# Kernel tuning notes

Measured on AMD Instinct MI355X. Metric: run time of the kernel, lower is better.

Reference implementation:

```python
import jax, jax.numpy as jnp
import numpy as np

MODEL_DIM = 2048
NUM_HEADS = 16
NUM_KV_HEADS = 4
HEAD_DIM = MODEL_DIM // NUM_HEADS  # 128
ROPE_BASE = 10000.0
LOCAL_WINDOW = 1024
EPS = 1.1920929e-07  # torch.finfo(float32).eps, F.rms_norm default
NEG = -1e30


def setup_inputs() -> dict:
    key = jax.random.key(0)
    ks = jax.random.split(key, 5)
    s = 0.02
    return {
        "x": jax.random.normal(ks[0], (1, 4096, MODEL_DIM), jnp.float32),
        "Wq": jax.random.normal(ks[1], (MODEL_DIM, MODEL_DIM), jnp.float32) * s,
        "Wk": jax.random.normal(ks[2], (NUM_KV_HEADS * HEAD_DIM, MODEL_DIM), jnp.float32) * s,
        "Wv": jax.random.normal(ks[3], (NUM_KV_HEADS * HEAD_DIM, MODEL_DIM), jnp.float32) * s,
        "Wo": jax.random.normal(ks[4], (MODEL_DIM, MODEL_DIM), jnp.float32) * s,
    }


def _rms_norm(x):
    return x * jax.lax.rsqrt(jnp.mean(x * x, axis=-1, keepdims=True) + EPS)


def _rope_tables(seqlen, dtype):
    inv_freq = 1.0 / (ROPE_BASE ** (jnp.arange(0, HEAD_DIM, 2, dtype=jnp.float32) / HEAD_DIM))
    freqs = jnp.arange(seqlen, dtype=jnp.float32)[:, None] * inv_freq[None, :]  # [S, hd/2]
    return jnp.cos(freqs).astype(dtype), jnp.sin(freqs).astype(dtype)


def _apply_rope(x, cos, sin):
    # x: [B, H, S, hd]; cos/sin: [S, hd/2]
    half = x.shape[-1] // 2
    x1, x2 = x[..., :half], x[..., half:]
    c = cos[None, None, :, :]
    s = sin[None, None, :, :]
    return jnp.concatenate((x1 * c + x2 * s, x2 * c - x1 * s), axis=-1)


def reference(x, Wq, Wk, Wv, Wo):
    B, S, _ = x.shape
    G = NUM_HEADS // NUM_KV_HEADS
    q = (x @ Wq.T).reshape(B, S, NUM_HEADS, HEAD_DIM).transpose(0, 2, 1, 3)
    k = (x @ Wk.T).reshape(B, S, NUM_KV_HEADS, HEAD_DIM).transpose(0, 2, 1, 3)
    v = (x @ Wv.T).reshape(B, S, NUM_KV_HEADS, HEAD_DIM).transpose(0, 2, 1, 3)
    q = _rms_norm(q)
    k = _rms_norm(k)
    cos, sin = _rope_tables(S, q.dtype)
    q = _apply_rope(q, cos, sin)
    k = _apply_rope(k, cos, sin)
    # GQA: expand kv heads to match query heads
    k = jnp.repeat(k, G, axis=1)  # [B, H, S, hd]
    v = jnp.repeat(v, G, axis=1)
    scale = 1.0 / np.sqrt(HEAD_DIM)
    scores = jnp.einsum("bhqd,bhkd->bhqk", q, k) * scale  # [B, H, S, S]
    idx = jnp.arange(S)
    causal = idx[None, :] <= idx[:, None]
    in_window = idx[None, :] > idx[:, None] - LOCAL_WINDOW
    allowed = causal & in_window  # [S, S]
    scores = jnp.where(allowed[None, None, :, :], scores, NEG)
    probs = jax.nn.softmax(scores, axis=-1)
    y = jnp.einsum("bhqk,bhkd->bhqd", probs, v)  # [B, H, S, hd]
    y = y.transpose(0, 2, 1, 3).reshape(B, S, MODEL_DIM)
    return y @ Wo.T
```

## Files before the change

### kernel.cpp

```cpp
#include <hip/hip_runtime.h>

typedef short bf16x8 __attribute__((ext_vector_type(8)));
typedef float f32x4 __attribute__((ext_vector_type(4)));

__device__ __forceinline__ ushort f2b(float f) {
  union { float f; unsigned u; } v; v.f = f;
  unsigned r = v.u + 0x7FFF + ((v.u >> 16) & 1);
  return (ushort)(r >> 16);
}
__device__ __forceinline__ float b2f(ushort u) {
  union { unsigned u; float f; } v; v.u = ((unsigned)u) << 16;
  return v.f;
}
__device__ __forceinline__ unsigned cvtpk(float lo, float hi) {
  unsigned r;
  asm volatile("v_cvt_pk_bf16_f32 %0, %1, %2" : "=v"(r) : "v"(lo), "v"(hi));
  return r;
}
__device__ __forceinline__ f32x4 mfma16(bf16x8 a, bf16x8 b, f32x4 c) {
  return __builtin_amdgcn_mfma_f32_16x16x32_bf16(a, b, c, 0, 0, 0);
}

#define GLD_LDS16(g, l) \
  __builtin_amdgcn_global_load_lds((const __attribute__((address_space(1))) void*)(g), \
                                   (__attribute__((address_space(3))) void*)(l), 16, 0, 0)

__global__ __launch_bounds__(256) void cast_all(const float* __restrict__ x,
                                                const float* __restrict__ wq,
                                                const float* __restrict__ wk,
                                                const float* __restrict__ wv,
                                                const float* __restrict__ wo,
                                                ushort* __restrict__ xb,
                                                ushort* __restrict__ wqkvb,
                                                ushort* __restrict__ wob) {
  const long i = (long)blockIdx.x * 256 + threadIdx.x;
  const float* src;
  ushort* dst;
  long j;
  if (i < 2097152) {
    src = x; j = i; dst = xb;
  } else if (i < 3145728) {
    src = wq; j = i - 2097152; dst = wqkvb;
  } else if (i < 3407872) {
    src = wk; j = i - 3145728; dst = wqkvb + 4194304;
  } else if (i < 3670016) {
    src = wv; j = i - 3407872; dst = wqkvb + 5242880;
  } else {
    src = wo; j = i - 3670016; dst = wob;
  }
  float4 f = ((const float4*)src)[j];
  ushort4 u;
  u.x = f2b(f.x); u.y = f2b(f.y); u.z = f2b(f.z); u.w = f2b(f.w);
  ((ushort4*)dst)[j] = u;
}

__global__ void rope_tables_k(float* __restrict__ cosT, float* __restrict__ sinT) {
  int s = blockIdx.x, i = threadIdx.x;
  float inv = powf(10000.0f, -(float)i * (1.0f / 64.0f));
  float f = (float)s * inv;
  cosT[s * 64 + i] = cosf(f);
  sinT[s * 64 + i] = sinf(f);
}

template <int BM, int BN, bool BF16OUT>
__global__ __launch_bounds__(512, 2) void gemm8p(const ushort* __restrict__ A,
                                                 const ushort* __restrict__ B,
                                                 void* __restrict__ Cout,
                                                 int M, int N, int K) {
  constexpr int AF = BM / 64;
  constexpr int BF = BN / 64;
  constexpr int MFR = BM / 32;
  constexpr int LA = BM / 128;
  constexpr int LB = BN / 128;
  constexpr int ASZ = BM * 32;
  constexpr int BSZ = BN * 32;
  constexpr int VMN = LA + 2 * LB;
  __shared__ __align__(16) ushort lds[4 * (ASZ + BSZ)];
  const int t = threadIdx.x;
  const int lane = t & 63, w = t >> 6;
  const int wr = w & 1, wc = w >> 1;
  const int l15 = lane & 15, l4 = lane >> 4;
  const int nbn = N / BN;
  const int nwg = (int)gridDim.x;
  int bid = (int)blockIdx.x;
  bid = (bid & 7) * (nwg >> 3) + (bid >> 3);
  const long m0 = (long)(bid / nbn) * BM;
  const long n0 = (long)(bid % nbn) * BN;
  const int nk = K >> 6;
  const int rdl = l15 * 32 + ((l4 ^ ((l15 >> 1) & 3)) * 8);

  f32x4 acc[MFR][BF] = {};
  bf16x8 af[AF], bf[BF];

#define STA(tile, ks)                                                          \
  do {                                                                         \
    const int tt_ = (tile) < nk ? (tile) : nk - 1;                             \
    _Pragma("unroll") for (int c = 0; c < LA; ++c) {                           \
      const int us_ = t * 8 + c * 4096;                                        \
      const int r_ = us_ >> 5;                                                 \
      const int cs_ = (((us_ >> 3) & 3) ^ ((r_ >> 1) & 3)) * 8;                \
      GLD_LDS16(A + (m0 + r_) * K + tt_ * 64 + (ks) * 32 + cs_,                \
                &lds[(((tile) & 1) * 2 + (ks)) * ASZ + us_]);                  \
    }                                                                          \
  } while (0)
#define STB(tile, ks)                                                          \
  do {                                                                         \
    const int tt_ = (tile) < nk ? (tile) : nk - 1;                             \
    _Pragma("unroll") for (int c = 0; c < LB; ++c) {                           \
      const int us_ = t * 8 + c * 4096;                                        \
      const int r_ = us_ >> 5;                                                 \
      const int cs_ = (((us_ >> 3) & 3) ^ ((r_ >> 1) & 3)) * 8;                \
      GLD_LDS16(B + (n0 + r_) * K + tt_ * 64 + (ks) * 32 + cs_,                \
                &lds[4 * ASZ + (((tile) & 1) * 2 + (ks)) * BSZ + us_]);        \
    }                                                                          \
  } while (0)
#define LDA8(slot, ks, mq)                                                     \
  _Pragma("unroll") for (int a = 0; a < AF; ++a)                               \
      af[a] = *(const bf16x8*)(&lds[((slot) * 2 + (ks)) * ASZ +                \
                                    (wr * MFR + (mq) * AF + a) * 512 + rdl]);
#define LDB8(slot, ks)                                                         \
  _Pragma("unroll") for (int b = 0; b < BF; ++b)                               \
      bf[b] = *(const bf16x8*)(&lds[4 * ASZ + ((slot) * 2 + (ks)) * BSZ +      \
                                    (wc * BF + b) * 512 + rdl]);
#define VMW()                                                                  \
  do {                                                                         \
    if constexpr (VMN == 7)                                                    \
      asm volatile("s_waitcnt vmcnt(7)" ::: "memory");                         \
    else if constexpr (VMN == 6)                                               \
      asm volatile("s_waitcnt vmcnt(6)" ::: "memory");                         \
    else                                                                       \
      asm volatile("s_waitcnt vmcnt(5)" ::: "memory");                         \
  } while (0)
#define BARMM(mq)                                                              \
  do {                                                                         \
    __builtin_amdgcn_s_barrier();                                              \
    asm volatile("s_waitcnt lgkmcnt(0)" ::: "memory");                         \
    __builtin_amdgcn_sched_barrier(0);                                         \
    __builtin_amdgcn_s_setprio(1);                                             \
    _Pragma("unroll") for (int a = 0; a < AF; ++a)                             \
        _Pragma("unroll") for (int b = 0; b < BF; ++b)                         \
            acc[(mq) * AF + a][b] = mfma16(af[a], bf[b], acc[(mq) * AF + a][b]); \
    __builtin_amdgcn_s_setprio(0);                                             \
    __builtin_amdgcn_s_barrier();                                              \
  } while (0)

  STA(0, 0); STB(0, 0); STA(0, 1); STB(0, 1);
  STA(1, 0); STB(1, 0); STB(1, 1);
  VMW();
  __builtin_amdgcn_s_barrier();

  for (int i = 0; i < (nk >> 1); ++i) {
    const int t1 = 2 * i + 1, t2 = 2 * i + 2, t3 = 2 * i + 3;
    LDA8(0, 0, 0); LDB8(0, 0); STA(t1, 1);          BARMM(0);
    LDA8(0, 0, 1);             STB(t2, 0);          BARMM(1);
    LDA8(0, 1, 0); LDB8(0, 1); STA(t2, 0);          BARMM(0);
    LDA8(0, 1, 1);             STB(t2, 1); VMW();   BARMM(1);
    LDA8(1, 0, 0); LDB8(1, 0); STA(t2, 1);          BARMM(0);
    LDA8(1, 0, 1);             STB(t3, 0);          BARMM(1);
    LDA8(1, 1, 0); LDB8(1, 1); STA(t3, 0);          BARMM(0);
    LDA8(1, 1, 1);             STB(t3, 1); VMW();   BARMM(1);
  }
  asm volatile("s_waitcnt vmcnt(0)" ::: "memory");

#pragma unroll
  for (int m = 0; m < MFR; ++m) {
#pragma unroll
    for (int n = 0; n < BF; ++n) {
      long mrow = m0 + wr * (BM / 2) + m * 16 + l4 * 4;
      long ncol = n0 + wc * (BN / 4) + n * 16 + l15;
#pragma unroll
      for (int r = 0; r < 4; ++r) {
        if constexpr (BF16OUT)
          ((ushort*)Cout)[(mrow + r) * N + ncol] = f2b(acc[m][n][r]);
        else
          ((float*)Cout)[(mrow + r) * N + ncol] = acc[m][n][r];
      }
    }
  }
#undef STA
#undef STB
#undef LDA8
#undef LDB8
#undef VMW
#undef BARMM
}

__global__ __launch_bounds__(256) void postproc_k(const ushort* __restrict__ qkvb,
                                                  const float* __restrict__ cosT,
                                                  const float* __restrict__ sinT,
                                                  ushort* __restrict__ qb,
                                                  ushort* __restrict__ kb,
                                                  ushort* __restrict__ vtb) {
  const int lane = threadIdx.x & 63;
  const int s = blockIdx.x * 4 + (threadIdx.x >> 6);
  const int h = blockIdx.y;
  const int colbase = (h < 16) ? h * 128 : (h < 20 ? 2048 + (h - 16) * 128
                                                   : 2560 + (h - 20) * 128);
  const ushort* row = qkvb + (long)s * 3072 + colbase;
  float x1 = b2f(row[lane]), x2 = b2f(row[lane + 64]);
  if (h >= 20) {
    int kvh = h - 20;
    int spos = (s & ~31) | (((s >> 2) & 3) * 8 + ((s >> 4) & 1) * 4 + (s & 3));
    vtb[(long)(kvh * 128 + lane) * 4096 + spos]      = f2b(x1);
    vtb[(long)(kvh * 128 + lane + 64) * 4096 + spos] = f2b(x2);
    return;
  }
  float ss = x1 * x1 + x2 * x2;
#pragma unroll
  for (int m = 1; m < 64; m <<= 1) ss += __shfl_xor(ss, m);
  float rn = rsqrtf(ss * (1.0f / 128.0f) + 1.1920929e-07f);
  float c = cosT[s * 64 + lane], sn = sinT[s * 64 + lane];
  float x1n = x1 * rn, x2n = x2 * rn;
  float o1 = x1n * c + x2n * sn;
  float o2 = x2n * c - x1n * sn;
  if (h < 16) {
    const float scq = 0.08838834764831845f;
    ushort* dst = qb + ((long)h * 4096 + s) * 128;
    dst[lane] = f2b(o1 * scq);
    dst[lane + 64] = f2b(o2 * scq);
  } else {
    ushort* dst = kb + ((long)(h - 16) * 4096 + s) * 128;
    dst[lane] = f2b(o1);
    dst[lane + 64] = f2b(o2);
  }
}

__global__ __launch_bounds__(256, 2) void attn_k(const ushort* __restrict__ qb,
                                                 const ushort* __restrict__ kb,
                                                 const ushort* __restrict__ vtb,
                                                 ushort* __restrict__ yb) {
  __shared__ __align__(16) ushort lds[32768];
  const int t = threadIdx.x;
  const int lane = t & 63, w = t >> 6;
  const int l15 = lane & 15, l4 = lane >> 4;
  const int q0 = ((int)gridDim.x - 1 - (int)blockIdx.x) * 128;
  const int h = blockIdx.y, kvh = h >> 2;
  const int qw = q0 + w * 32;
  const int qA = qw + l15, qB = qw + 16 + l15;
  const int lrd = l15 * 32 + ((l4 ^ ((l15 >> 1) & 3)) * 8);

  bf16x8 qf0[4], qf1[4];
  {
    const ushort* QpA = qb + ((long)h * 4096 + qA) * 128 + l4 * 8;
    const ushort* QpB = qb + ((long)h * 4096 + qB) * 128 + l4 * 8;
#pragma unroll
    for (int c = 0; c < 4; ++c) {
      qf0[c] = *(const bf16x8*)(QpA + c * 32);
      qf1[c] = *(const bf16x8*)(QpB + c * 32);
    }
  }

  const ushort* Kg = kb + (long)kvh * 4096 * 128;
  const ushort* Vg = vtb + (long)kvh * 128 * 4096;

  int kb_lo = q0 - 1023; if (kb_lo < 0) kb_lo = 0; kb_lo &= ~63;
  const int nt = (q0 + 127 - kb_lo) / 64 + 1;

#define STAGE(kbs, b)                                                          \
  do {                                                                         \
    ushort* L_ = &lds[(b) * 16384];                                            \
    _Pragma("unroll") for (int c = 0; c < 8; ++c) {                            \
      const int us_ = t * 8 + c * 2048;                                        \
      if (c < 4) {                                                             \
        const int r_ = (us_ >> 5) & 63;                                        \
        const int cs_ = (((us_ >> 3) & 3) ^ ((r_ >> 1) & 3)) * 8;              \
        GLD_LDS16(Kg + (long)((kbs) + r_) * 128 + (us_ >> 11) * 32 + cs_,      \
                  L_ + us_);                                                   \
      } else {                                                                 \
        const int uv_ = us_ - 8192;                                            \
        const int r_ = (uv_ >> 5) & 127;                                       \
        const int cs_ = (((uv_ >> 3) & 3) ^ ((r_ >> 1) & 3)) * 8;              \
        GLD_LDS16(Vg + (long)r_ * 4096 + (kbs) + (uv_ >> 12) * 32 + cs_,       \
                  L_ + us_);                                                   \
      }                                                                        \
    }                                                                          \
  } while (0)

#define SMAX(sg, mr, lr, og, PA, PB)                                           \
  do {                                                                         \
    float mx = fmaxf(fmaxf(fmaxf(sg[0], sg[1]), fmaxf(sg[2], sg[3])),          \
                     fmaxf(fmaxf(sg[4], sg[5]), fmaxf(sg[6], sg[7])));         \
    mx = fmaxf(mx, fmaxf(fmaxf(fmaxf(sg[8], sg[9]), fmaxf(sg[10], sg[11])),    \
                         fmaxf(fmaxf(sg[12], sg[13]), fmaxf(sg[14], sg[15]))));\
    mx = fmaxf(mx, __shfl_xor(mx, 16));                                        \
    mx = fmaxf(mx, __shfl_xor(mx, 32));                                        \
    float mn;                                                                  \
    if (__all(mx <= (mr) + 8.0f)) {                                            \
      mn = (mr);                                                               \
    } else {                                                                   \
      mn = fmaxf((mr), mx);                                                    \
      const float corr = __expf((mr)-mn);                                      \
      (mr) = mn;                                                               \
      _Pragma("unroll") for (int db = 0; db < 8; ++db)                         \
          _Pragma("unroll") for (int r = 0; r < 4; ++r) og[db][r] *= corr;     \
      (lr) *= corr;                                                            \
    }                                                                          \
    float p[16];                                                               \
    _Pragma("unroll") for (int j = 0; j < 16; ++j) p[j] = __expf(sg[j] - mn);  \
    float ps = ((p[0] + p[1]) + (p[2] + p[3])) + ((p[4] + p[5]) + (p[6] + p[7])); \
    ps += ((p[8] + p[9]) + (p[10] + p[11])) + ((p[12] + p[13]) + (p[14] + p[15])); \
    ps += __shfl_xor(ps, 16);                                                  \
    ps += __shfl_xor(ps, 32);                                                  \
    (lr) += ps;                                                                \
    PA.u[0] = cvtpk(p[0], p[1]);   PA.u[1] = cvtpk(p[2], p[3]);                \
    PA.u[2] = cvtpk(p[4], p[5]);   PA.u[3] = cvtpk(p[6], p[7]);                \
    PB.u[0] = cvtpk(p[8], p[9]);   PB.u[1] = cvtpk(p[10], p[11]);              \
    PB.u[2] = cvtpk(p[12], p[13]); PB.u[3] = cvtpk(p[14], p[15]);              \
  } while (0)

  f32x4 o0[8] = {}, o1[8] = {};
  float mr0 = -1e30f, lr0 = 0.0f, mr1 = -1e30f, lr1 = 0.0f;

  STAGE(kb_lo, 0);

  for (int ti = 0; ti < nt; ++ti) {
    const int kbs = kb_lo + ti * 64;
    const int cur = ti & 1;
    const int tn = (ti + 1 < nt) ? ti + 1 : nt - 1;
    STAGE(kb_lo + tn * 64, cur ^ 1);
    asm volatile("s_waitcnt vmcnt(8)" ::: "memory");
    __builtin_amdgcn_s_barrier();

    if (kbs <= qw + 31 && kbs + 63 >= qw - 1023) {
      const ushort* Kl = &lds[cur * 16384];
      const ushort* Vl = Kl + 8192;

      f32x4 sc0[4], sc1[4];
#pragma unroll
      for (int st = 0; st < 4; ++st) {
        sc0[st] = f32x4{0.f, 0.f, 0.f, 0.f};
        sc1[st] = f32x4{0.f, 0.f, 0.f, 0.f};
#pragma unroll
        for (int c = 0; c < 4; ++c) {
          bf16x8 kf = *(const bf16x8*)(Kl + c * 2048 + st * 512 + lrd);
          sc0[st] = mfma16(kf, qf0[c], sc0[st]);
          sc1[st] = mfma16(kf, qf1[c], sc1[st]);
        }
      }

      float s0[16], s1[16];
      const bool fullA = (kbs + 64 <= qw) && (kbs >= qw - 1008);
      const bool fullB = (kbs + 64 <= qw + 16) && (kbs >= qw - 992);
      if (fullA) {
#pragma unroll
        for (int st = 0; st < 4; ++st)
#pragma unroll
          for (int r = 0; r < 4; ++r) s0[st * 4 + r] = sc0[st][r];
      } else {
#pragma unroll
        for (int st = 0; st < 4; ++st)
#pragma unroll
          for (int r = 0; r < 4; ++r) {
            const int ki = kbs + st * 16 + l4 * 4 + r;
            s0[st * 4 + r] = (ki <= qA && ki > qA - 1024) ? sc0[st][r] : -1e30f;
          }
      }
      if (fullB) {
#pragma unroll
        for (int st = 0; st < 4; ++st)
#pragma unroll
          for (int r = 0; r < 4; ++r) s1[st * 4 + r] = sc1[st][r];
      } else {
#pragma unroll
        for (int st = 0; st < 4; ++st)
#pragma unroll
          for (int r = 0; r < 4; ++r) {
            const int ki = kbs + st * 16 + l4 * 4 + r;
            s1[st * 4 + r] = (ki <= qB && ki > qB - 1024) ? sc1[st][r] : -1e30f;
          }
      }

      union { unsigned u[4]; bf16x8 v; } pa0, pb0, pa1, pb1;
      SMAX(s0, mr0, lr0, o0, pa0, pb0);
      SMAX(s1, mr1, lr1, o1, pa1, pb1);

#pragma unroll
      for (int db = 0; db < 8; ++db) {
        bf16x8 v0 = *(const bf16x8*)(Vl + db * 512 + lrd);
        o0[db] = mfma16(v0, pa0.v, o0[db]);
        o1[db] = mfma16(v0, pa1.v, o1[db]);
        bf16x8 v1 = *(const bf16x8*)(Vl + 4096 + db * 512 + lrd);
        o0[db] = mfma16(v1, pb0.v, o0[db]);
        o1[db] = mfma16(v1, pb1.v, o1[db]);
      }
    }
    __builtin_amdgcn_s_barrier();
  }

  const float i0 = 1.0f / lr0, i1 = 1.0f / lr1;
#pragma unroll
  for (int db = 0; db < 8; ++db)
#pragma unroll
    for (int r = 0; r < 4; ++r) {
      yb[(long)qA * 2048 + h * 128 + db * 16 + l4 * 4 + r] = f2b(o0[db][r] * i0);
      yb[(long)qB * 2048 + h * 128 + db * 16 + l4 * 4 + r] = f2b(o1[db][r] * i1);
    }
#undef STAGE
#undef SMAX
}

extern "C" void kernel_launch(void* const* d_in, const int* in_sizes, int n_in,
                              void* d_out, int out_size, void* d_ws, size_t ws_size,
                              hipStream_t stream) {
  (void)in_sizes; (void)n_in; (void)out_size; (void)ws_size;
  const float* x  = (const float*)d_in[0];
  const float* Wq = (const float*)d_in[1];
  const float* Wk = (const float*)d_in[2];
  const float* Wv = (const float*)d_in[3];
  const float* Wo = (const float*)d_in[4];
  const long S = 4096;
  ushort* ws   = (ushort*)d_ws;
  ushort* xb   = ws;
  ushort* wqkv = xb + S * 2048;
  ushort* wob  = wqkv + 3072L * 2048;
  ushort* qkvb = wob + 2048L * 2048;
  ushort* qb   = qkvb + S * 3072;
  ushort* kbuf = qb + S * 2048;
  ushort* vtb  = kbuf + 4L * 4096 * 128;
  ushort* yb   = vtb + 4L * 128 * 4096;
  float* cosT  = (float*)(yb + S * 2048);
  float* sinT  = cosT + S * 64;

  cast_all<<<dim3(18432), 256, 0, stream>>>(x, Wq, Wk, Wv, Wo, xb, wqkv, wob);
  gemm8p<128, 384, true><<<dim3(256), 512, 0, stream>>>(xb, wqkv, qkvb, 4096, 3072, 2048);
  rope_tables_k<<<dim3(4096), 64, 0, stream>>>(cosT, sinT);
  postproc_k<<<dim3(1024, 24), 256, 0, stream>>>(qkvb, cosT, sinT, qb, kbuf, vtb);
  attn_k<<<dim3(32, 16), 256, 0, stream>>>(qb, kbuf, vtb, yb);
  gemm8p<128, 256, false><<<dim3(256), 512, 0, stream>>>(yb, wob, d_out, 4096, 2048, 2048);
}
```

Measured before the change: 191.0 us.

## Enlarge attention query tile to 256 rows, four 16-row groups per wave

Each attention block now covers 256 query rows instead of 128, and each wave handles four 16-row query groups instead of two. Every K/V tile staged into LDS is reused by twice as many queries, which halves the K/V global traffic and the LDS reads per query. The grid shrinks from 512 to 256 blocks, and the per-thread accumulator and Q-fragment registers double. The launch bound drops its 2-blocks-per-SM hint, so occupancy and load balance across the mi355x's CUs may suffer.

```diff
diff --git a/kernel.cpp b/kernel.cpp
--- a/kernel.cpp
+++ b/kernel.cpp
@@ -225,36 +225,32 @@
   }
 }
 
-__global__ __launch_bounds__(256, 2) void attn_k(const ushort* __restrict__ qb,
-                                                 const ushort* __restrict__ kb,
-                                                 const ushort* __restrict__ vtb,
-                                                 ushort* __restrict__ yb) {
+__global__ __launch_bounds__(256) void attn_k(const ushort* __restrict__ qb,
+                                              const ushort* __restrict__ kb,
+                                              const ushort* __restrict__ vtb,
+                                              ushort* __restrict__ yb) {
   __shared__ __align__(16) ushort lds[32768];
   const int t = threadIdx.x;
   const int lane = t & 63, w = t >> 6;
   const int l15 = lane & 15, l4 = lane >> 4;
-  const int q0 = ((int)gridDim.x - 1 - (int)blockIdx.x) * 128;
+  const int q0 = ((int)gridDim.x - 1 - (int)blockIdx.x) * 256;
   const int h = blockIdx.y, kvh = h >> 2;
-  const int qw = q0 + w * 32;
-  const int qA = qw + l15, qB = qw + 16 + l15;
+  const int qw = q0 + w * 64;
   const int lrd = l15 * 32 + ((l4 ^ ((l15 >> 1) & 3)) * 8);
 
-  bf16x8 qf0[4], qf1[4];
-  {
-    const ushort* QpA = qb + ((long)h * 4096 + qA) * 128 + l4 * 8;
-    const ushort* QpB = qb + ((long)h * 4096 + qB) * 128 + l4 * 8;
-#pragma unroll
-    for (int c = 0; c < 4; ++c) {
-      qf0[c] = *(const bf16x8*)(QpA + c * 32);
-      qf1[c] = *(const bf16x8*)(QpB + c * 32);
-    }
+  bf16x8 qf[4][4];
+#pragma unroll
+  for (int g = 0; g < 4; ++g) {
+    const ushort* Qp = qb + ((long)h * 4096 + qw + g * 16 + l15) * 128 + l4 * 8;
+#pragma unroll
+    for (int c = 0; c < 4; ++c) qf[g][c] = *(const bf16x8*)(Qp + c * 32);
   }
 
   const ushort* Kg = kb + (long)kvh * 4096 * 128;
   const ushort* Vg = vtb + (long)kvh * 128 * 4096;
 
   int kb_lo = q0 - 1023; if (kb_lo < 0) kb_lo = 0; kb_lo &= ~63;
-  const int nt = (q0 + 127 - kb_lo) / 64 + 1;
+  const int nt = (q0 + 255 - kb_lo) / 64 + 1;
 
 #define STAGE(kbs, b)                                                          \
   do {                                                                         \
@@ -276,7 +272,7 @@
     }                                                                          \
   } while (0)
 
-#define SMAX(sg, mr, lr, og, PA, PB)                                           \
+#define SMAX(sg, mr_, lr_, og, PA, PB)                                         \
   do {                                                                         \
     float mx = fmaxf(fmaxf(fmaxf(sg[0], sg[1]), fmaxf(sg[2], sg[3])),          \
                      fmaxf(fmaxf(sg[4], sg[5]), fmaxf(sg[6], sg[7])));         \
@@ -285,15 +281,15 @@
     mx = fmaxf(mx, __shfl_xor(mx, 16));                                        \
     mx = fmaxf(mx, __shfl_xor(mx, 32));                                        \
     float mn;                                                                  \
-    if (__all(mx <= (mr) + 8.0f)) {                                            \
-      mn = (mr);                                                               \
+    if (__all(mx <= (mr_) + 8.0f)) {                                           \
+      mn = (mr_);                                                              \
     } else {                                                                   \
-      mn = fmaxf((mr), mx);                                                    \
-      const float corr = __expf((mr)-mn);                                      \
-      (mr) = mn;                                                               \
+      mn = fmaxf((mr_), mx);                                                   \
+      const float corr = __expf((mr_)-mn);                                     \
+      (mr_) = mn;                                                              \
       _Pragma("unroll") for (int db = 0; db < 8; ++db)                         \
           _Pragma("unroll") for (int r = 0; r < 4; ++r) og[db][r] *= corr;     \
-      (lr) *= corr;                                                            \
+      (lr_) *= corr;                                                           \
     }                                                                          \
     float p[16];                                                               \
     _Pragma("unroll") for (int j = 0; j < 16; ++j) p[j] = __expf(sg[j] - mn);  \
@@ -301,15 +297,18 @@
     ps += ((p[8] + p[9]) + (p[10] + p[11])) + ((p[12] + p[13]) + (p[14] + p[15])); \
     ps += __shfl_xor(ps, 16);                                                  \
     ps += __shfl_xor(ps, 32);                                                  \
-    (lr) += ps;                                                                \
+    (lr_) += ps;                                                               \
     PA.u[0] = cvtpk(p[0], p[1]);   PA.u[1] = cvtpk(p[2], p[3]);                \
     PA.u[2] = cvtpk(p[4], p[5]);   PA.u[3] = cvtpk(p[6], p[7]);                \
     PB.u[0] = cvtpk(p[8], p[9]);   PB.u[1] = cvtpk(p[10], p[11]);              \
     PB.u[2] = cvtpk(p[12], p[13]); PB.u[3] = cvtpk(p[14], p[15]);              \
   } while (0)
 
-  f32x4 o0[8] = {}, o1[8] = {};
-  float mr0 = -1e30f, lr0 = 0.0f, mr1 = -1e30f, lr1 = 0.0f;
+  f32x4 o[4][8] = {};
+  float mr[4], lr[4];
+#pragma unroll
+  for (int g = 0; g < 4; ++g) { mr[g] = -1e30f; lr[g] = 0.0f; }
+  union PU { unsigned u[4]; bf16x8 v; };
 
   STAGE(kb_lo, 0);
 
@@ -321,80 +320,72 @@
     asm volatile("s_waitcnt vmcnt(8)" ::: "memory");
     __builtin_amdgcn_s_barrier();
 
-    if (kbs <= qw + 31 && kbs + 63 >= qw - 1023) {
+    if (kbs <= qw + 63 && kbs + 63 >= qw - 1023) {
       const ushort* Kl = &lds[cur * 16384];
       const ushort* Vl = Kl + 8192;
 
-      f32x4 sc0[4], sc1[4];
+      f32x4 sc[4][4];
+#pragma unroll
+      for (int g = 0; g < 4; ++g)
+#pragma unroll
+        for (int st = 0; st < 4; ++st) sc[g][st] = f32x4{0.f, 0.f, 0.f, 0.f};
 #pragma unroll
       for (int st = 0; st < 4; ++st) {
-        sc0[st] = f32x4{0.f, 0.f, 0.f, 0.f};
-        sc1[st] = f32x4{0.f, 0.f, 0.f, 0.f};
 #pragma unroll
         for (int c = 0; c < 4; ++c) {
           bf16x8 kf = *(const bf16x8*)(Kl + c * 2048 + st * 512 + lrd);
-          sc0[st] = mfma16(kf, qf0[c], sc0[st]);
-          sc1[st] = mfma16(kf, qf1[c], sc1[st]);
+#pragma unroll
+          for (int g = 0; g < 4; ++g) sc[g][st] = mfma16(kf, qf[g][c], sc[g][st]);
         }
       }
 
-      float s0[16], s1[16];
-      const bool fullA = (kbs + 64 <= qw) && (kbs >= qw - 1008);
-      const bool fullB = (kbs + 64 <= qw + 16) && (kbs >= qw - 992);
-      if (fullA) {
-#pragma unroll
-        for (int st = 0; st < 4; ++st)
-#pragma unroll
-          for (int r = 0; r < 4; ++r) s0[st * 4 + r] = sc0[st][r];
-      } else {
-#pragma unroll
-        for (int st = 0; st < 4; ++st)
-#pragma unroll
-          for (int r = 0; r < 4; ++r) {
-            const int ki = kbs + st * 16 + l4 * 4 + r;
-            s0[st * 4 + r] = (ki <= qA && ki > qA - 1024) ? sc0[st][r] : -1e30f;
-          }
+      PU pa[4], pb[4];
+#pragma unroll
+      for (int g = 0; g < 4; ++g) {
+        const int qg0 = qw + g * 16;
+        const int qg = qg0 + l15;
+        float s[16];
+        if ((kbs + 64 <= qg0) && (kbs >= qg0 - 1008)) {
+#pragma unroll
+          for (int st = 0; st < 4; ++st)
+#pragma unroll
+            for (int r = 0; r < 4; ++r) s[st * 4 + r] = sc[g][st][r];
+        } else {
+#pragma unroll
+          for (int st = 0; st < 4; ++st)
+#pragma unroll
+            for (int r = 0; r < 4; ++r) {
+              const int ki = kbs + st * 16 + l4 * 4 + r;
+              s[st * 4 + r] = (ki <= qg && ki > qg - 1024) ? sc[g][st][r] : -1e30f;
+            }
+        }
+        SMAX(s, mr[g], lr[g], o[g], pa[g], pb[g]);
       }
-      if (fullB) {
-#pragma unroll
-        for (int st = 0; st < 4; ++st)
-#pragma unroll
-          for (int r = 0; r < 4; ++r) s1[st * 4 + r] = sc1[st][r];
-      } else {
-#pragma unroll
-        for (int st = 0; st < 4; ++st)
-#pragma unroll
-          for (int r = 0; r < 4; ++r) {
-            const int ki = kbs + st * 16 + l4 * 4 + r;
-            s1[st * 4 + r] = (ki <= qB && ki > qB - 1024) ? sc1[st][r] : -1e30f;
-          }
-      }
-
-      union { unsigned u[4]; bf16x8 v; } pa0, pb0, pa1, pb1;
-      SMAX(s0, mr0, lr0, o0, pa0, pb0);
-      SMAX(s1, mr1, lr1, o1, pa1, pb1);
 
 #pragma unroll
       for (int db = 0; db < 8; ++db) {
         bf16x8 v0 = *(const bf16x8*)(Vl + db * 512 + lrd);
-        o0[db] = mfma16(v0, pa0.v, o0[db]);
-        o1[db] = mfma16(v0, pa1.v, o1[db]);
         bf16x8 v1 = *(const bf16x8*)(Vl + 4096 + db * 512 + lrd);
-        o0[db] = mfma16(v1, pb0.v, o0[db]);
-        o1[db] = mfma16(v1, pb1.v, o1[db]);
+#pragma unroll
+        for (int g = 0; g < 4; ++g) {
+          o[g][db] = mfma16(v0, pa[g].v, o[g][db]);
+          o[g][db] = mfma16(v1, pb[g].v, o[g][db]);
+        }
       }
     }
     __builtin_amdgcn_s_barrier();
   }
 
-  const float i0 = 1.0f / lr0, i1 = 1.0f / lr1;
-#pragma unroll
-  for (int db = 0; db < 8; ++db)
-#pragma unroll
-    for (int r = 0; r < 4; ++r) {
-      yb[(long)qA * 2048 + h * 128 + db * 16 + l4 * 4 + r] = f2b(o0[db][r] * i0);
-      yb[(long)qB * 2048 + h * 128 + db * 16 + l4 * 4 + r] = f2b(o1[db][r] * i1);
-    }
+#pragma unroll
+  for (int g = 0; g < 4; ++g) {
+    const float inv = 1.0f / lr[g];
+    const long qrow = qw + g * 16 + l15;
+#pragma unroll
+    for (int db = 0; db < 8; ++db)
+#pragma unroll
+      for (int r = 0; r < 4; ++r)
+        yb[qrow * 2048 + h * 128 + db * 16 + l4 * 4 + r] = f2b(o[g][db][r] * inv);
+  }
 #undef STAGE
 #undef SMAX
 }
@@ -425,6 +416,6 @@
   gemm8p<128, 384, true><<<dim3(256), 512, 0, stream>>>(xb, wqkv, qkvb, 4096, 3072, 2048);
   rope_tables_k<<<dim3(4096), 64, 0, stream>>>(cosT, sinT);
   postproc_k<<<dim3(1024, 24), 256, 0, stream>>>(qkvb, cosT, sinT, qb, kbuf, vtb);
-  attn_k<<<dim3(32, 16), 256, 0, stream>>>(qb, kbuf, vtb, yb);
+  attn_k<<<dim3(16, 16), 256, 0, stream>>>(qb, kbuf, vtb, yb);
   gemm8p<128, 256, false><<<dim3(256), 512, 0, stream>>>(yb, wob, d_out, 4096, 2048, 2048);
 }
```

New measurement: 224.3 us. 1.17x slower.

## Load V fragments directly from global memory instead of staging through LDS

Applied to the files above, without the earlier changes.

Only K tiles are now staged in LDS, which halves the shared buffer. Each wave loads its V^T fragments straight from global memory into registers, and the loads are interleaved with the softmax to hide their latency. The launch-bounds occupancy hint is dropped and the vmcnt wait is lowered to match the smaller staging. Every wave now fetches the same V data separately, so global/L2 traffic and register pressure go up in exchange for lower LDS usage and fewer LDS reads.

```diff
diff --git a/kernel.cpp b/kernel.cpp
--- a/kernel.cpp
+++ b/kernel.cpp
@@ -225,11 +225,11 @@
   }
 }
 
-__global__ __launch_bounds__(256, 2) void attn_k(const ushort* __restrict__ qb,
-                                                 const ushort* __restrict__ kb,
-                                                 const ushort* __restrict__ vtb,
-                                                 ushort* __restrict__ yb) {
-  __shared__ __align__(16) ushort lds[32768];
+__global__ __launch_bounds__(256) void attn_k(const ushort* __restrict__ qb,
+                                              const ushort* __restrict__ kb,
+                                              const ushort* __restrict__ vtb,
+                                              ushort* __restrict__ yb) {
+  __shared__ __align__(16) ushort lds[16384];
   const int t = threadIdx.x;
   const int lane = t & 63, w = t >> 6;
   const int l15 = lane & 15, l4 = lane >> 4;
@@ -258,21 +258,13 @@
 
 #define STAGE(kbs, b)                                                          \
   do {                                                                         \
-    ushort* L_ = &lds[(b) * 16384];                                            \
-    _Pragma("unroll") for (int c = 0; c < 8; ++c) {                            \
+    ushort* L_ = &lds[(b) * 8192];                                             \
+    _Pragma("unroll") for (int c = 0; c < 4; ++c) {                            \
       const int us_ = t * 8 + c * 2048;                                        \
-      if (c < 4) {                                                             \
-        const int r_ = (us_ >> 5) & 63;                                        \
-        const int cs_ = (((us_ >> 3) & 3) ^ ((r_ >> 1) & 3)) * 8;              \
-        GLD_LDS16(Kg + (long)((kbs) + r_) * 128 + (us_ >> 11) * 32 + cs_,      \
-                  L_ + us_);                                                   \
-      } else {                                                                 \
-        const int uv_ = us_ - 8192;                                            \
-        const int r_ = (uv_ >> 5) & 127;                                       \
-        const int cs_ = (((uv_ >> 3) & 3) ^ ((r_ >> 1) & 3)) * 8;              \
-        GLD_LDS16(Vg + (long)r_ * 4096 + (kbs) + (uv_ >> 12) * 32 + cs_,       \
-                  L_ + us_);                                                   \
-      }                                                                        \
+      const int r_ = (us_ >> 5) & 63;                                          \
+      const int cs_ = (((us_ >> 3) & 3) ^ ((r_ >> 1) & 3)) * 8;                \
+      GLD_LDS16(Kg + (long)((kbs) + r_) * 128 + (us_ >> 11) * 32 + cs_,        \
+                L_ + us_);                                                     \
     }                                                                          \
   } while (0)
 
@@ -318,12 +310,11 @@
     const int cur = ti & 1;
     const int tn = (ti + 1 < nt) ? ti + 1 : nt - 1;
     STAGE(kb_lo + tn * 64, cur ^ 1);
-    asm volatile("s_waitcnt vmcnt(8)" ::: "memory");
+    asm volatile("s_waitcnt vmcnt(4)" ::: "memory");
     __builtin_amdgcn_s_barrier();
 
     if (kbs <= qw + 31 && kbs + 63 >= qw - 1023) {
-      const ushort* Kl = &lds[cur * 16384];
-      const ushort* Vl = Kl + 8192;
+      const ushort* Kl = &lds[cur * 8192];
 
       f32x4 sc0[4], sc1[4];
 #pragma unroll
@@ -338,6 +329,11 @@
         }
       }
 
+      bf16x8 v0[8];
+#pragma unroll
+      for (int db = 0; db < 8; ++db)
+        v0[db] = *(const bf16x8*)(Vg + (long)(db * 16 + l15) * 4096 + kbs + l4 * 8);
+
       float s0[16], s1[16];
       const bool fullA = (kbs + 64 <= qw) && (kbs >= qw - 1008);
       const bool fullB = (kbs + 64 <= qw + 16) && (kbs >= qw - 992);
@@ -372,16 +368,23 @@
 
       union { unsigned u[4]; bf16x8 v; } pa0, pb0, pa1, pb1;
       SMAX(s0, mr0, lr0, o0, pa0, pb0);
+
+      bf16x8 v1[8];
+#pragma unroll
+      for (int db = 0; db < 8; ++db)
+        v1[db] = *(const bf16x8*)(Vg + (long)(db * 16 + l15) * 4096 + kbs + 32 + l4 * 8);
+
       SMAX(s1, mr1, lr1, o1, pa1, pb1);
 
 #pragma unroll
       for (int db = 0; db < 8; ++db) {
-        bf16x8 v0 = *(const bf16x8*)(Vl + db * 512 + lrd);
-        o0[db] = mfma16(v0, pa0.v, o0[db]);
-        o1[db] = mfma16(v0, pa1.v, o1[db]);
-        bf16x8 v1 = *(const bf16x8*)(Vl + 4096 + db * 512 + lrd);
-        o0[db] = mfma16(v1, pb0.v, o0[db]);
-        o1[db] = mfma16(v1, pb1.v, o1[db]);
+        o0[db] = mfma16(v0[db], pa0.v, o0[db]);
+        o1[db] = mfma16(v0[db], pa1.v, o1[db]);
+      }
+#pragma unroll
+      for (int db = 0; db < 8; ++db) {
+        o0[db] = mfma16(v1[db], pb0.v, o0[db]);
+        o1[db] = mfma16(v1[db], pb1.v, o1[db]);
       }
     }
     __builtin_amdgcn_s_barrier();
```

New measurement: 243.9 us. +27.7%, slower.
